# Kernel optimization log

Hardware: AMD Instinct MI355X
Metric: run time of the kernel (lower is better)

The kernel has to match this reference:

```python
import jax, jax.numpy as jnp
import numpy as np

B, D, C, F = 1024, 8192, 345, 512
PROTO_W = 0.99  # args.proto_m


def setup_inputs() -> dict:
    key = jax.random.key(0)
    k = jax.random.split(key, 6)
    img_q = jax.random.normal(k[0], (B, D), jnp.float32)
    img_q1 = jax.random.normal(k[1], (B, D), jnp.float32)
    # partial label mask: random candidate set, guarantee >=1 candidate per row
    partial_Y = (jax.random.uniform(k[2], (B, C)) < 0.3).astype(jnp.float32)
    partial_Y = partial_Y.at[jnp.arange(B), jnp.arange(B) % C].set(1.0)
    W_enc = jax.random.normal(k[3], (D, F), jnp.float32) / np.sqrt(D).astype(np.float32)
    W_fc = jax.random.normal(k[4], (F, C), jnp.float32) / np.sqrt(F).astype(np.float32)
    b_fc = jnp.zeros((C,), jnp.float32)
    proto = jax.random.normal(k[5], (C, F), jnp.float32)
    proto = proto / jnp.linalg.norm(proto, axis=1, keepdims=True)
    return {"img_q": img_q, "img_q1": img_q1, "partial_Y": partial_Y,
            "W_enc": W_enc, "W_fc": W_fc, "b_fc": b_fc, "proto": proto}


def reference(img_q, img_q1, partial_Y, W_enc, W_fc, b_fc, proto):
    # encoder: feats [B,F], logits [B,C] (abstracted backbone + shared fc)
    feats_q = img_q @ W_enc
    logits_q = feats_q @ W_fc + b_fc
    feats_q1 = img_q1 @ W_enc
    logits_q1 = feats_q1 @ W_fc + b_fc

    # partial-label restricted pseudo labels
    scores = jax.nn.softmax(logits_q, axis=1) * partial_Y
    scores = scores / scores.sum(axis=1, keepdims=True)
    labels = jnp.argmax(scores, axis=1)  # [B] int

    # Sequential per-sample EMA p[l] = w*p[l] + (1-w)*f, vectorized in closed form.
    # For a sample with c_after same-label samples occurring later, its final
    # contribution is (1-w)*w^c_after * f; the old prototype is scaled by w^count.
    onehot = jax.nn.one_hot(labels, C, dtype=feats_q.dtype)   # [B,C]
    cum = jnp.cumsum(onehot, axis=0)                          # inclusive counts
    occ = cum[jnp.arange(B), labels] - 1.0                    # occurrences before i
    total = cum[-1]                                           # [C] per-class counts
    c_after = total[labels] - occ - 1.0                       # [B]
    coef = (1.0 - PROTO_W) * PROTO_W ** c_after               # [B]
    contrib = jax.ops.segment_sum(coef[:, None] * feats_q, labels, num_segments=C)
    new_proto = (PROTO_W ** total)[:, None] * proto + contrib
    new_proto = new_proto / jnp.linalg.norm(new_proto, axis=1, keepdims=True)

    prot_scores = new_proto @ W_fc + b_fc
    return logits_q, logits_q1, new_proto, prot_scores, labels, feats_q, feats_q1
```

## Files before the change

### kernel.cpp

```cpp
#include <hip/hip_runtime.h>
#include <float.h>
#include <math.h>

#define B_SZ 1024
#define D_SZ 8192
#define C_SZ 345
#define F_SZ 512
#define PROTO_W 0.99f


#define WS_XH 0
#define WS_XL 33554432u
#define WS_WH 67108864u
#define WS_WL 75497472u
#define WS_P  83886080u
#define WS2_WFH 100663296u
#define WS2_WFL 101056512u
#define WS2_LAB 101449728u
#define WS2_NEED 101457920u

#define WS_NEED 92274688u
#define WS_FH  0u
#define WS_FL  2097152u
#define WS_WFH 4194304u
#define WS_WFL 4587520u
#define WS_NPH 4980736u
#define WS_NPL 5373952u

typedef short bf16x8 __attribute__((ext_vector_type(8)));
typedef short short4v __attribute__((ext_vector_type(4)));
typedef short short8v __attribute__((ext_vector_type(8)));
typedef float f32x4  __attribute__((ext_vector_type(4)));

__device__ __forceinline__ void split_bf16(float x, short& hi, short& lo) {
    unsigned u = __float_as_uint(x);
    unsigned r = (u + 0x7FFFu + ((u >> 16) & 1u)) >> 16;
    hi = (short)r;
    float hf = __uint_as_float(r << 16);
    lo = (short)(__float_as_uint(x - hf) >> 16);
}
__device__ __forceinline__ float bf16_f32(short h) {
    return __uint_as_float(((unsigned)(unsigned short)h) << 16);
}

__device__ __forceinline__ void gl_lds16(const short* g, short* l) {
    __builtin_amdgcn_global_load_lds(
        (const __attribute__((address_space(1))) void*)g,
        (__attribute__((address_space(3))) void*)l, 16, 0, 0);
}

__device__ __forceinline__ unsigned f2key(float v) {
    unsigned u = __float_as_uint(v);
    return (u & 0x80000000u) ? ~u : (u | 0x80000000u);
}

#define MFMA_BF16 __builtin_amdgcn_mfma_f32_16x16x32_bf16

#define MFMA_BLOCK(IA0, IA1, IB0, IB1)                                   \
    do {                                                                 \
        bf16x8 a0h = *(const bf16x8*)&sAh[IA0];                          \
        bf16x8 a1h = *(const bf16x8*)&sAh[IA1];                          \
        bf16x8 b0h = *(const bf16x8*)&sBh[IB0];                          \
        bf16x8 b1h = *(const bf16x8*)&sBh[IB1];                          \
        bf16x8 a0l = *(const bf16x8*)&sAl[IA0];                          \
        bf16x8 a1l = *(const bf16x8*)&sAl[IA1];                          \
        bf16x8 b0l = *(const bf16x8*)&sBl[IB0];                          \
        bf16x8 b1l = *(const bf16x8*)&sBl[IB1];                          \
        acc[0][0] = MFMA_BF16(a0h, b0h, acc[0][0], 0, 0, 0);             \
        acc[0][1] = MFMA_BF16(a0h, b1h, acc[0][1], 0, 0, 0);             \
        acc[1][0] = MFMA_BF16(a1h, b0h, acc[1][0], 0, 0, 0);             \
        acc[1][1] = MFMA_BF16(a1h, b1h, acc[1][1], 0, 0, 0);             \
        acc[0][0] = MFMA_BF16(a0h, b0l, acc[0][0], 0, 0, 0);             \
        acc[0][1] = MFMA_BF16(a0h, b1l, acc[0][1], 0, 0, 0);             \
        acc[1][0] = MFMA_BF16(a1h, b0l, acc[1][0], 0, 0, 0);             \
        acc[1][1] = MFMA_BF16(a1h, b1l, acc[1][1], 0, 0, 0);             \
        acc[0][0] = MFMA_BF16(a0l, b0h, acc[0][0], 0, 0, 0);             \
        acc[0][1] = MFMA_BF16(a0l, b1h, acc[0][1], 0, 0, 0);             \
        acc[1][0] = MFMA_BF16(a1l, b0h, acc[1][0], 0, 0, 0);             \
        acc[1][1] = MFMA_BF16(a1l, b1h, acc[1][1], 0, 0, 0);             \
    } while (0)

__global__ __launch_bounds__(256) void convert_all(
    const float* __restrict__ img_q, const float* __restrict__ img_q1,
    const float* __restrict__ W_enc, const float* __restrict__ W_fc,
    short* __restrict__ Xh, short* __restrict__ Xl,
    short* __restrict__ Wh, short* __restrict__ Wl,
    short* __restrict__ Wth, short* __restrict__ Wtl)
{
    __shared__ float tile[64][65];
    const int bid = blockIdx.x;
    const int t = threadIdx.x;

    if (bid < 1024) {
        const int HALF = (B_SZ * D_SZ) / 4;
        const int total = 2 * HALF;
        for (int i4 = bid * 256 + t; i4 < total; i4 += 1024 * 256) {
            float4 v = (i4 < HALF) ? ((const float4*)img_q)[i4]
                                   : ((const float4*)img_q1)[i4 - HALF];
            short4v h, l;
            short hh, ll;
            split_bf16(v.x, hh, ll); h.x = hh; l.x = ll;
            split_bf16(v.y, hh, ll); h.y = hh; l.y = ll;
            split_bf16(v.z, hh, ll); h.z = hh; l.z = ll;
            split_bf16(v.w, hh, ll); h.w = hh; l.w = ll;
            ((short4v*)Xh)[i4] = h;
            ((short4v*)Xl)[i4] = l;
        }
    } else if (bid < 2048) {
        const int id = bid - 1024;
        const int k0 = (id >> 3) * 64;
        const int n0 = (id & 7) * 64;
        {
            const int kr = t >> 2;
            const int cb = (t & 3) * 16;
#pragma unroll
            for (int j = 0; j < 4; ++j) {
                float4 v = *(const float4*)&W_enc[(size_t)(k0 + kr) * F_SZ + n0 + cb + j * 4];
                tile[kr][cb + j * 4 + 0] = v.x;
                tile[kr][cb + j * 4 + 1] = v.y;
                tile[kr][cb + j * 4 + 2] = v.z;
                tile[kr][cb + j * 4 + 3] = v.w;
            }
        }
        __syncthreads();
        const int n = t >> 2;
#pragma unroll
        for (int cc = 0; cc < 2; ++cc) {
            const int ch = (t & 3) * 2 + cc;
            short8v h, l;
#pragma unroll
            for (int e = 0; e < 8; ++e) {
                short hh, ll;
                split_bf16(tile[ch * 8 + e][n], hh, ll);
                h[e] = hh; l[e] = ll;
            }
            size_t off = (size_t)(n0 + n) * D_SZ + k0 + ch * 8;
            *(short8v*)&Wh[off] = h;
            *(short8v*)&Wl[off] = l;
        }
    } else {
        const int id = bid - 2048;
        const int k0 = (id & 7) * 64;
        const int c0 = (id >> 3) * 64;
        for (int idx = t; idx < 64 * 64; idx += 256) {
            const int kr = idx >> 6;
            const int cc = idx & 63;
            tile[kr][cc] = (c0 + cc < C_SZ) ? W_fc[(size_t)(k0 + kr) * C_SZ + c0 + cc] : 0.0f;
        }
        __syncthreads();
        const int crow = t >> 2;
#pragma unroll
        for (int cc2 = 0; cc2 < 2; ++cc2) {
            const int ch = (t & 3) * 2 + cc2;
            short8v h, l;
#pragma unroll
            for (int e = 0; e < 8; ++e) {
                short hh, ll;
                split_bf16(tile[ch * 8 + e][crow], hh, ll);
                h[e] = hh; l[e] = ll;
            }
            size_t off = (size_t)(c0 + crow) * F_SZ + k0 + ch * 8;
            *(short8v*)&Wth[off] = h;
            *(short8v*)&Wtl[off] = l;
        }
    }
}

__global__ __launch_bounds__(256, 1) void gemm_ws128(
    const short* __restrict__ Xh, const short* __restrict__ Xl,
    const short* __restrict__ Wh, const short* __restrict__ Wl,
    float* __restrict__ P, int ksteps)
{
    __shared__ __align__(16) short sAh[2][8192];
    __shared__ __align__(16) short sAl[2][8192];
    __shared__ __align__(16) short sBh[2][8192];
    __shared__ __align__(16) short sBl[2][8192];

    const int t = threadIdx.x;
    const int lane = t & 63;
    const int wave = t >> 6;
    const int nt = blockIdx.x;
    const int mt = blockIdx.y;
    const int ks = blockIdx.z;
    const int m0 = mt * 128;
    const int n0 = nt * 128;
    const int kbase = ks * ksteps * 64;

    const short* gbase =
        (wave == 0) ? Xh + (size_t)m0 * D_SZ :
        (wave == 1) ? Xl + (size_t)m0 * D_SZ :
        (wave == 2) ? Wh + (size_t)n0 * D_SZ :
                      Wl + (size_t)n0 * D_SZ;
    short* lb[2];
    lb[0] = (wave == 0) ? sAh[0] : (wave == 1) ? sAl[0] : (wave == 2) ? sBh[0] : sBl[0];
    lb[1] = (wave == 0) ? sAh[1] : (wave == 1) ? sAl[1] : (wave == 2) ? sBh[1] : sBl[1];
    const int lrow8 = lane >> 3;
    const int gchunkOff = ((lane & 7) ^ lrow8) * 8;
    const short* gsrc = gbase + (size_t)lrow8 * D_SZ + kbase + gchunkOff;

    const int mo = (wave >> 1) * 64;
    const int no = (wave & 1) * 64;
    const int lr = lane & 15;
    const int lkg = lane >> 4;
    const int x7 = lr & 7;
    const int sl0 = lkg ^ x7;
    const int sl1 = (4 + lkg) ^ x7;
    int aoff[4], boff[4];
#pragma unroll
    for (int f = 0; f < 4; ++f) {
        aoff[f] = (mo + 16 * f + lr) * 64;
        boff[f] = (no + 16 * f + lr) * 64;
    }

    f32x4 acc[4][4] = {};

#pragma unroll
    for (int j = 0; j < 16; ++j)
        gl_lds16(gsrc + (size_t)(8 * j) * D_SZ, lb[0] + j * 512);
    __syncthreads();

    int buf = 0;
    for (int s = 0; s < ksteps; ++s) {
        if (s + 1 < ksteps) {
            short* dst = lb[buf ^ 1];
            const short* g = gsrc + (s + 1) * 64;
#pragma unroll
            for (int j = 0; j < 16; ++j)
                gl_lds16(g + (size_t)(8 * j) * D_SZ, dst + j * 512);
        }
        const short* pAh = sAh[buf];
        const short* pAl = sAl[buf];
        const short* pBh = sBh[buf];
        const short* pBl = sBl[buf];
#pragma unroll
        for (int ksub = 0; ksub < 2; ++ksub) {
            const int sl = ksub ? sl1 : sl0;
            bf16x8 ah[4], al[4], bh[4], blo[4];
#pragma unroll
            for (int f = 0; f < 4; ++f) {
                ah[f]  = *(const bf16x8*)&pAh[aoff[f] + sl * 8];
                al[f]  = *(const bf16x8*)&pAl[aoff[f] + sl * 8];
            }
#pragma unroll
            for (int g = 0; g < 4; ++g) {
                bh[g]  = *(const bf16x8*)&pBh[boff[g] + sl * 8];
                blo[g] = *(const bf16x8*)&pBl[boff[g] + sl * 8];
            }
#pragma unroll
            for (int f = 0; f < 4; ++f)
#pragma unroll
                for (int g = 0; g < 4; ++g)
                    acc[f][g] = MFMA_BF16(ah[f], bh[g], acc[f][g], 0, 0, 0);
#pragma unroll
            for (int f = 0; f < 4; ++f)
#pragma unroll
                for (int g = 0; g < 4; ++g)
                    acc[f][g] = MFMA_BF16(ah[f], blo[g], acc[f][g], 0, 0, 0);
#pragma unroll
            for (int f = 0; f < 4; ++f)
#pragma unroll
                for (int g = 0; g < 4; ++g)
                    acc[f][g] = MFMA_BF16(al[f], bh[g], acc[f][g], 0, 0, 0);
        }
        __syncthreads();
        buf ^= 1;
    }

    float* Pout = P + (size_t)ks * (2048u * 512u);
#pragma unroll
    for (int f = 0; f < 4; ++f)
#pragma unroll
        for (int g = 0; g < 4; ++g) {
            const int col  = n0 + no + 16 * g + (lane & 15);
            const int row0 = m0 + mo + 16 * f + (lane >> 4) * 4;
#pragma unroll
            for (int r = 0; r < 4; ++r)
                Pout[(size_t)(row0 + r) * F_SZ + col] = acc[f][g][r];
        }
}

__global__ __launch_bounds__(256) void fc_logits_fused2(
    const float* __restrict__ P,
    const short* __restrict__ Bh_g, const short* __restrict__ Bl_g,
    const float* __restrict__ bias, const float* __restrict__ partial_Y,
    float* __restrict__ logits, float* __restrict__ feats,
    unsigned long long* __restrict__ labPack)
{
    __shared__ __align__(16) short sAh[4096];
    __shared__ __align__(16) short sAl[4096];
    __shared__ __align__(16) short sBh[4096];
    __shared__ __align__(16) short sBl[4096];

    const int t = threadIdx.x;
    const int lane = t & 63;
    const int wave = t >> 6;
    const int n0 = blockIdx.x * 64;
    const int m0 = blockIdx.y * 64;
    const bool writeF = (blockIdx.x == 0);

    const int lrow8 = lane >> 3;
    const int colOff = ((lane & 7) ^ lrow8) * 8;

    const int mo = (wave >> 1) * 32;
    const int no = (wave & 1) * 32;
    const int lr = lane & 15;
    const int lkg = lane >> 4;
    const int x7 = lr & 7;
    const int sl0 = (0 + lkg) ^ x7;
    const int sl1 = (4 + lkg) ^ x7;
    const int ra0 = (mo + lr) * 64,      ra1 = (mo + 16 + lr) * 64;
    const int rb0 = (no + lr) * 64,      rb1 = (no + 16 + lr) * 64;
    const int a00 = ra0 + sl0 * 8, a01 = ra0 + sl1 * 8;
    const int a10 = ra1 + sl0 * 8, a11 = ra1 + sl1 * 8;
    const int b00 = rb0 + sl0 * 8, b01 = rb0 + sl1 * 8;
    const int b10 = rb1 + sl0 * 8, b11 = rb1 + sl1 * 8;

    f32x4 acc[2][2] = {};

    for (int s = 0; s < 8; ++s) {
        __syncthreads();
        if (wave < 2) {
            const short* gB = (wave == 0) ? Bh_g : Bl_g;
            short* lbase = (wave == 0) ? sBh : sBl;
#pragma unroll
            for (int j = 0; j < 8; ++j) {
                int row = n0 + lrow8 + 8 * j;
                gl_lds16(gB + (size_t)row * F_SZ + s * 64 + colOff, lbase + j * 512);
            }
        }
#pragma unroll
        for (int qq = 0; qq < 2; ++qq) {
            const int q = t + qq * 256;
            const int row = q >> 3;
            const int c = q & 7;
            const size_t gidx = (size_t)(m0 + row) * F_SZ + s * 64 + c * 8;
            float4 v0 = ((const float4*)&P[gidx])[0];
            float4 v1 = ((const float4*)&P[gidx])[1];
#pragma unroll
            for (int sl = 1; sl < 4; ++sl) {
                const float* Ps = P + (size_t)sl * (2048u * 512u);
                float4 u0 = ((const float4*)&Ps[gidx])[0];
                float4 u1 = ((const float4*)&Ps[gidx])[1];
                v0.x += u0.x; v0.y += u0.y; v0.z += u0.z; v0.w += u0.w;
                v1.x += u1.x; v1.y += u1.y; v1.z += u1.z; v1.w += u1.w;
            }
            float f[8] = {v0.x, v0.y, v0.z, v0.w, v1.x, v1.y, v1.z, v1.w};
            if (writeF) {
#pragma unroll
                for (int e = 0; e < 8; ++e) feats[gidx + e] = f[e];
            }
            bf16x8 h, l;
#pragma unroll
            for (int e = 0; e < 8; ++e) { short hh, ll; split_bf16(f[e], hh, ll); h[e] = hh; l[e] = ll; }
            const int slot = c ^ (row & 7);
            *(bf16x8*)&sAh[row * 64 + slot * 8] = h;
            *(bf16x8*)&sAl[row * 64 + slot * 8] = l;
        }
        __syncthreads();
        MFMA_BLOCK(a00, a10, b00, b10);
        MFMA_BLOCK(a01, a11, b01, b11);
    }

    const bool doArg = (m0 < B_SZ);
#pragma unroll
    for (int f = 0; f < 2; ++f) {
#pragma unroll
        for (int r = 0; r < 4; ++r) {
            const int row = m0 + mo + f * 16 + (lane >> 4) * 4 + r;
            unsigned long long best = 0;
#pragma unroll
            for (int g = 0; g < 2; ++g) {
                const int col = n0 + no + g * 16 + (lane & 15);
                if (col < C_SZ) {
                    const float v = acc[f][g][r] + bias[col];
                    logits[(size_t)row * C_SZ + col] = v;
                    if (doArg && partial_Y[(size_t)row * C_SZ + col] != 0.0f) {
                        unsigned long long p = ((unsigned long long)f2key(v) << 32)
                                             | (unsigned long long)(0xFFFFFFFFu - (unsigned)col);
                        if (p > best) best = p;
                    }
                }
            }
            if (doArg) {
#pragma unroll
                for (int m = 1; m < 16; m <<= 1) {
                    unsigned long long o = __shfl_xor(best, m);
                    if (o > best) best = o;
                }
                if ((lane & 15) == 0 && best != 0)
                    atomicMax(&labPack[row], best);
            }
        }
    }
}

__global__ __launch_bounds__(512) void proto_scores_fused(
    const unsigned long long* __restrict__ labPack,
    const float* __restrict__ feats_q,
    const float* __restrict__ proto,
    const short* __restrict__ Wth, const short* __restrict__ Wtl,
    const float* __restrict__ b_fc,
    float* __restrict__ new_proto, float* __restrict__ scores,
    float* __restrict__ labels_f)
{
    __shared__ int rowlist[B_SZ];
    __shared__ int mcount_s;
    __shared__ float nprow[F_SZ];
    __shared__ float red[8];
    __shared__ float rinv_s;
    const int c = blockIdx.x;
    const int t = threadIdx.x;
    const int lane = t & 63;
    const int w = t >> 6;

    if (c == 0) {
#pragma unroll
        for (int j = 0; j < 2; ++j) {
            const int i = t + j * 512;
            int li = (int)(0xFFFFFFFFu - (unsigned)(labPack[i] & 0xFFFFFFFFull));
            labels_f[i] = (float)li;
        }
    }

    if (w == 0) {
        int k = 0;
#pragma unroll
        for (int ch = 0; ch < 16; ++ch) {
            unsigned long long pk = labPack[ch * 64 + lane];
            int li = (int)(0xFFFFFFFFu - (unsigned)(pk & 0xFFFFFFFFull));
            unsigned long long mask = __ballot(li == c);
            if (lane == 0) {
                while (mask) {
                    int p = __builtin_ctzll(mask);
                    mask &= mask - 1;
                    rowlist[k++] = ch * 64 + p;
                }
            }
            k = __shfl(k, 0);
        }
        if (lane == 0) mcount_s = k;
    }
    __syncthreads();
    const int m = mcount_s;

    float val = proto[(size_t)c * F_SZ + t];
    for (int k = 0; k < m; ++k)
        val = PROTO_W * val + (1.0f - PROTO_W) * feats_q[(size_t)rowlist[k] * F_SZ + t];

    float sq = val * val;
#pragma unroll
    for (int off = 32; off; off >>= 1) sq += __shfl_down(sq, off);
    if ((t & 63) == 0) red[t >> 6] = sq;
    __syncthreads();
    if (t == 0) {
        float s = 0.0f;
#pragma unroll
        for (int ww = 0; ww < 8; ++ww) s += red[ww];
        rinv_s = 1.0f / sqrtf(s);
    }
    __syncthreads();
    const float v = val * rinv_s;
    new_proto[(size_t)c * F_SZ + t] = v;
    nprow[t] = v;
    __syncthreads();

    float np8[8];
#pragma unroll
    for (int j = 0; j < 8; ++j) np8[j] = nprow[lane * 8 + j];
    for (int col = w; col < C_SZ; col += 8) {
        const short8v h = *(const short8v*)&Wth[(size_t)col * F_SZ + lane * 8];
        const short8v l = *(const short8v*)&Wtl[(size_t)col * F_SZ + lane * 8];
        float p = 0.0f;
#pragma unroll
        for (int j = 0; j < 8; ++j)
            p += np8[j] * (bf16_f32(h[j]) + bf16_f32(l[j]));
#pragma unroll
        for (int off = 32; off; off >>= 1) p += __shfl_down(p, off);
        if (lane == 0) scores[(size_t)c * C_SZ + col] = p + b_fc[col];
    }
}

__global__ __launch_bounds__(256) void reduce_feats_split(
    const float* __restrict__ P, float* __restrict__ feats,
    short* __restrict__ Fh, short* __restrict__ Fl,
    const float* __restrict__ W_fc,
    short* __restrict__ Wth, short* __restrict__ Wtl)
{
    const int bid = blockIdx.x;
    const int t = threadIdx.x;
    if (bid < 1024) {
        const int n4 = (2048 * 512) / 4;
        const float* P1 = P + 2048 * 512;
        for (int i4 = bid * 256 + t; i4 < n4; i4 += 1024 * 256) {
            float4 a = ((const float4*)P)[i4];
            float4 b = ((const float4*)P1)[i4];
            float v[4] = {a.x + b.x, a.y + b.y, a.z + b.z, a.w + b.w};
            short4v h, l;
            short hh, ll;
#pragma unroll
            for (int e = 0; e < 4; ++e) {
                feats[i4 * 4 + e] = v[e];
                split_bf16(v[e], hh, ll); h[e] = hh; l[e] = ll;
            }
            ((short4v*)Fh)[i4] = h;
            ((short4v*)Fl)[i4] = l;
        }
    } else {
        __shared__ float tile[64][65];
        const int id = bid - 1024;
        const int k0 = (id & 7) * 64;
        const int c0 = (id >> 3) * 64;
        for (int idx = t; idx < 64 * 64; idx += 256) {
            const int kr = idx >> 6;
            const int cc = idx & 63;
            tile[kr][cc] = (c0 + cc < C_SZ) ? W_fc[(size_t)(k0 + kr) * C_SZ + c0 + cc] : 0.0f;
        }
        __syncthreads();
        const int crow = t >> 2;
#pragma unroll
        for (int cc2 = 0; cc2 < 2; ++cc2) {
            const int ch = (t & 3) * 2 + cc2;
            short8v h, l;
#pragma unroll
            for (int e = 0; e < 8; ++e) {
                short hh, ll;
                split_bf16(tile[ch * 8 + e][crow], hh, ll);
                h[e] = hh; l[e] = ll;
            }
            size_t off = (size_t)(c0 + crow) * F_SZ + k0 + ch * 8;
            *(short8v*)&Wth[off] = h;
            *(short8v*)&Wtl[off] = l;
        }
    }
}

__global__ __launch_bounds__(256) void gemm_fc(
    const short* __restrict__ Ah, const short* __restrict__ Al,
    const short* __restrict__ Bh, const short* __restrict__ Bl,
    const float* __restrict__ bias, float* __restrict__ Cout, int M)
{
    __shared__ __align__(16) short sAh[4096];
    __shared__ __align__(16) short sAl[4096];
    __shared__ __align__(16) short sBh[4096];
    __shared__ __align__(16) short sBl[4096];

    const int t = threadIdx.x;
    const int lane = t & 63;
    const int wave = t >> 6;
    const int n0 = blockIdx.x * 64;
    const int m0 = blockIdx.y * 64;

    const int lrow8 = lane >> 3;
    const int colOff = ((lane & 7) ^ lrow8) * 8;

    short* lbase = (wave == 0) ? sAh : (wave == 1) ? sAl : (wave == 2) ? sBh : sBl;
    const short* gA = (wave == 1) ? Al : Ah;
    const short* gB = (wave == 3) ? Bl : Bh;
    const bool isA = wave < 2;

    const int mo = (wave >> 1) * 32;
    const int no = (wave & 1) * 32;
    const int lr = lane & 15;
    const int lkg = lane >> 4;
    const int x7 = lr & 7;
    const int sl0 = (0 + lkg) ^ x7;
    const int sl1 = (4 + lkg) ^ x7;
    const int ra0 = (mo + lr) * 64,      ra1 = (mo + 16 + lr) * 64;
    const int rb0 = (no + lr) * 64,      rb1 = (no + 16 + lr) * 64;
    const int a00 = ra0 + sl0 * 8, a01 = ra0 + sl1 * 8;
    const int a10 = ra1 + sl0 * 8, a11 = ra1 + sl1 * 8;
    const int b00 = rb0 + sl0 * 8, b01 = rb0 + sl1 * 8;
    const int b10 = rb1 + sl0 * 8, b11 = rb1 + sl1 * 8;

    f32x4 acc[2][2] = {};

    for (int s = 0; s < 8; ++s) {
        __syncthreads();
        if (isA) {
#pragma unroll
            for (int j = 0; j < 8; ++j) {
                int row = m0 + lrow8 + 8 * j;
                if (row > M - 1) row = M - 1;
                gl_lds16(gA + (size_t)row * F_SZ + s * 64 + colOff, lbase + j * 512);
            }
        } else {
#pragma unroll
            for (int j = 0; j < 8; ++j) {
                int row = n0 + lrow8 + 8 * j;
                gl_lds16(gB + (size_t)row * F_SZ + s * 64 + colOff, lbase + j * 512);
            }
        }
        __syncthreads();
        MFMA_BLOCK(a00, a10, b00, b10);
        MFMA_BLOCK(a01, a11, b01, b11);
    }

#pragma unroll
    for (int f = 0; f < 2; ++f)
#pragma unroll
        for (int g = 0; g < 2; ++g) {
            const int col  = n0 + no + g * 16 + (lane & 15);
            if (col >= C_SZ) continue;
            const float bb = bias[col];
            const int row0 = m0 + mo + f * 16 + (lane >> 4) * 4;
#pragma unroll
            for (int r = 0; r < 4; ++r) {
                const int row = row0 + r;
                if (row < M)
                    Cout[(size_t)row * C_SZ + col] = acc[f][g][r] + bb;
            }
        }
}

__global__ __launch_bounds__(64) void argmax_labels(
    const float* __restrict__ logits, const float* __restrict__ partial_Y,
    float* __restrict__ labels_f)
{
    const int i = blockIdx.x;
    const int lane = threadIdx.x;
    float best = -FLT_MAX;
    int bidx = C_SZ;
    for (int c = lane; c < C_SZ; c += 64) {
        if (partial_Y[(size_t)i * C_SZ + c] != 0.0f) {
            float v = logits[(size_t)i * C_SZ + c];
            if (v > best || (v == best && c < bidx)) { best = v; bidx = c; }
        }
    }
#pragma unroll
    for (int off = 32; off; off >>= 1) {
        float ov = __shfl_down(best, off);
        int oi = __shfl_down(bidx, off);
        if (ov > best || (ov == best && oi < bidx)) { best = ov; bidx = oi; }
    }
    if (lane == 0) labels_f[i] = (float)bidx;
}

__global__ __launch_bounds__(512) void proto_update(
    const float* __restrict__ labels_f, const float* __restrict__ feats_q,
    const float* __restrict__ proto, float* __restrict__ new_proto,
    short* __restrict__ NPh, short* __restrict__ NPl)
{
    __shared__ int lab[B_SZ];
    __shared__ float red[8];
    __shared__ float rinv_s;
    const int c = blockIdx.x;
    const int t = threadIdx.x;
    for (int i = t; i < B_SZ; i += 512) lab[i] = (int)labels_f[i];
    __syncthreads();
    float val = proto[(size_t)c * F_SZ + t];
    for (int i = 0; i < B_SZ; ++i) {
        if (lab[i] == c)
            val = PROTO_W * val + (1.0f - PROTO_W) * feats_q[(size_t)i * F_SZ + t];
    }
    float sq = val * val;
#pragma unroll
    for (int off = 32; off; off >>= 1) sq += __shfl_down(sq, off);
    if ((t & 63) == 0) red[t >> 6] = sq;
    __syncthreads();
    if (t == 0) {
        float s = 0.0f;
#pragma unroll
        for (int w = 0; w < 8; ++w) s += red[w];
        rinv_s = 1.0f / sqrtf(s);
    }
    __syncthreads();
    const float v = val * rinv_s;
    new_proto[(size_t)c * F_SZ + t] = v;
    if (NPh) {
        short hh, ll;
        split_bf16(v, hh, ll);
        NPh[(size_t)c * F_SZ + t] = hh;
        NPl[(size_t)c * F_SZ + t] = ll;
    }
}

extern "C" void kernel_launch(void* const* d_in, const int* in_sizes, int n_in,
                              void* d_out, int out_size, void* d_ws, size_t ws_size,
                              hipStream_t stream)
{
    const float* img_q     = (const float*)d_in[0];
    const float* img_q1    = (const float*)d_in[1];
    const float* partial_Y = (const float*)d_in[2];
    const float* W_enc     = (const float*)d_in[3];
    const float* W_fc      = (const float*)d_in[4];
    const float* b_fc      = (const float*)d_in[5];
    const float* proto     = (const float*)d_in[6];

    float* out       = (float*)d_out;
    float* logits    = out;
    float* new_proto = out + 706560;
    float* scores    = out + 883200;
    float* labels_f  = out + 1002225;
    float* feats     = out + 1003249;

    char* ws = (char*)d_ws;
    short* Xh = (short*)(ws + WS_XH);
    short* Xl = (short*)(ws + WS_XL);
    short* Wh = (short*)(ws + WS_WH);
    short* Wl = (short*)(ws + WS_WL);
    float* P  = (float*)(ws + WS_P);

    if (ws_size >= (size_t)WS2_NEED) {
        short* Wth = (short*)(ws + WS2_WFH);
        short* Wtl = (short*)(ws + WS2_WFL);
        unsigned long long* labPack = (unsigned long long*)(ws + WS2_LAB);

        hipMemsetAsync(labPack, 0, B_SZ * sizeof(unsigned long long), stream);
        hipLaunchKernelGGL(convert_all, dim3(2096), dim3(256), 0, stream,
                           img_q, img_q1, W_enc, W_fc, Xh, Xl, Wh, Wl, Wth, Wtl);
        hipLaunchKernelGGL(gemm_ws128, dim3(4, 16, 4), dim3(256), 0, stream,
                           Xh, Xl, Wh, Wl, P, 32);
        hipLaunchKernelGGL(fc_logits_fused2, dim3(6, 32), dim3(256), 0, stream,
                           P, Wth, Wtl, b_fc, partial_Y, logits, feats, labPack);
        hipLaunchKernelGGL(proto_scores_fused, dim3(345), dim3(512), 0, stream,
                           labPack, feats, proto, Wth, Wtl, b_fc,
                           new_proto, scores, labels_f);
    } else {
        short* Fh  = (short*)(ws + WS_FH);
        short* Fl  = (short*)(ws + WS_FL);
        short* Wth = (short*)(ws + WS_WFH);
        short* Wtl = (short*)(ws + WS_WFL);
        short* NPh = (short*)(ws + WS_NPH);
        short* NPl = (short*)(ws + WS_NPL);

        hipLaunchKernelGGL(convert_all, dim3(2048), dim3(256), 0, stream,
                           img_q, img_q1, W_enc, W_fc, Xh, Xl, Wh, Wl,
                           (short*)nullptr, (short*)nullptr);
        hipLaunchKernelGGL(gemm_ws128, dim3(4, 16, 2), dim3(256), 0, stream,
                           Xh, Xl, Wh, Wl, P, 64);
        hipLaunchKernelGGL(reduce_feats_split, dim3(1072), dim3(256), 0, stream,
                           P, feats, Fh, Fl, W_fc, Wth, Wtl);
        hipLaunchKernelGGL(gemm_fc, dim3(6, 32), dim3(256), 0, stream,
                           Fh, Fl, Wth, Wtl, b_fc, logits, 2048);
        hipLaunchKernelGGL(argmax_labels, dim3(1024), dim3(64), 0, stream,
                           logits, partial_Y, labels_f);
        hipLaunchKernelGGL(proto_update, dim3(345), dim3(512), 0, stream,
                           labels_f, feats, proto, new_proto, NPh, NPl);
        hipLaunchKernelGGL(gemm_fc, dim3(6, 6), dim3(256), 0, stream,
                           NPh, NPl, Wth, Wtl, b_fc, scores, C_SZ);
    }
}
```

Measured before the change: 257.1 us.

## Split out split-K reduction and double-buffer the fc GEMM with async LDS loads

Moves the split-K partial-sum reduction and bf16 hi/lo split into a separate reduce_feats4 kernel. Previously every column block of the fc kernel re-read and re-summed all four partial slices of P. The new fc_logits3 kernel streams precomputed Fh/Fl tiles with global-to-LDS loads into double buffers. The main split-K GEMM swaps __syncthreads for explicit vmcnt waits plus raw barriers and raises wave priority around the MFMA section, so prefetch overlaps compute. This costs one extra kernel launch and a 4 MB round-trip through workspace, and it doubles LDS use in the fc kernel.

```diff
diff --git a/kernel.cpp b/kernel.cpp
--- a/kernel.cpp
+++ b/kernel.cpp
@@ -18,6 +18,8 @@
 #define WS2_WFL 101056512u
 #define WS2_LAB 101449728u
 #define WS2_NEED 101457920u
+#define WS2_FH 0u
+#define WS2_FL 2097152u
 
 #define WS_NEED 92274688u
 #define WS_FH  0u
@@ -52,6 +54,12 @@
 __device__ __forceinline__ unsigned f2key(float v) {
     unsigned u = __float_as_uint(v);
     return (u & 0x80000000u) ? ~u : (u | 0x80000000u);
+}
+
+__device__ __forceinline__ void fence_barrier() {
+    asm volatile("" ::: "memory");
+    __builtin_amdgcn_s_barrier();
+    asm volatile("" ::: "memory");
 }
 
 #define MFMA_BF16 __builtin_amdgcn_mfma_f32_16x16x32_bf16
@@ -217,7 +225,6 @@
 #pragma unroll
     for (int j = 0; j < 16; ++j)
         gl_lds16(gsrc + (size_t)(8 * j) * D_SZ, lb[0] + j * 512);
-    __syncthreads();
 
     int buf = 0;
     for (int s = 0; s < ksteps; ++s) {
@@ -227,42 +234,51 @@
 #pragma unroll
             for (int j = 0; j < 16; ++j)
                 gl_lds16(g + (size_t)(8 * j) * D_SZ, dst + j * 512);
-        }
-        const short* pAh = sAh[buf];
-        const short* pAl = sAl[buf];
-        const short* pBh = sBh[buf];
-        const short* pBl = sBl[buf];
-#pragma unroll
-        for (int ksub = 0; ksub < 2; ++ksub) {
-            const int sl = ksub ? sl1 : sl0;
-            bf16x8 ah[4], al[4], bh[4], blo[4];
-#pragma unroll
-            for (int f = 0; f < 4; ++f) {
-                ah[f]  = *(const bf16x8*)&pAh[aoff[f] + sl * 8];
-                al[f]  = *(const bf16x8*)&pAl[aoff[f] + sl * 8];
-            }
-#pragma unroll
-            for (int g = 0; g < 4; ++g) {
-                bh[g]  = *(const bf16x8*)&pBh[boff[g] + sl * 8];
-                blo[g] = *(const bf16x8*)&pBl[boff[g] + sl * 8];
-            }
-#pragma unroll
-            for (int f = 0; f < 4; ++f)
-#pragma unroll
-                for (int g = 0; g < 4; ++g)
-                    acc[f][g] = MFMA_BF16(ah[f], bh[g], acc[f][g], 0, 0, 0);
-#pragma unroll
-            for (int f = 0; f < 4; ++f)
-#pragma unroll
-                for (int g = 0; g < 4; ++g)
-                    acc[f][g] = MFMA_BF16(ah[f], blo[g], acc[f][g], 0, 0, 0);
-#pragma unroll
-            for (int f = 0; f < 4; ++f)
-#pragma unroll
-                for (int g = 0; g < 4; ++g)
-                    acc[f][g] = MFMA_BF16(al[f], bh[g], acc[f][g], 0, 0, 0);
-        }
-        __syncthreads();
+            asm volatile("s_waitcnt vmcnt(16)" ::: "memory");
+        } else {
+            asm volatile("s_waitcnt vmcnt(0)" ::: "memory");
+        }
+        fence_barrier();
+
+        __builtin_amdgcn_s_setprio(1);
+        {
+            const short* pAh = sAh[buf];
+            const short* pAl = sAl[buf];
+            const short* pBh = sBh[buf];
+            const short* pBl = sBl[buf];
+#pragma unroll
+            for (int ksub = 0; ksub < 2; ++ksub) {
+                const int sl = ksub ? sl1 : sl0;
+                bf16x8 ah[4], al[4], bh[4], blo[4];
+#pragma unroll
+                for (int f = 0; f < 4; ++f) {
+                    ah[f]  = *(const bf16x8*)&pAh[aoff[f] + sl * 8];
+                    al[f]  = *(const bf16x8*)&pAl[aoff[f] + sl * 8];
+                }
+#pragma unroll
+                for (int g = 0; g < 4; ++g) {
+                    bh[g]  = *(const bf16x8*)&pBh[boff[g] + sl * 8];
+                    blo[g] = *(const bf16x8*)&pBl[boff[g] + sl * 8];
+                }
+#pragma unroll
+                for (int f = 0; f < 4; ++f)
+#pragma unroll
+                    for (int g = 0; g < 4; ++g)
+                        acc[f][g] = MFMA_BF16(ah[f], bh[g], acc[f][g], 0, 0, 0);
+#pragma unroll
+                for (int f = 0; f < 4; ++f)
+#pragma unroll
+                    for (int g = 0; g < 4; ++g)
+                        acc[f][g] = MFMA_BF16(ah[f], blo[g], acc[f][g], 0, 0, 0);
+#pragma unroll
+                for (int f = 0; f < 4; ++f)
+#pragma unroll
+                    for (int g = 0; g < 4; ++g)
+                        acc[f][g] = MFMA_BF16(al[f], bh[g], acc[f][g], 0, 0, 0);
+            }
+        }
+        __builtin_amdgcn_s_setprio(0);
+        fence_barrier();
         buf ^= 1;
     }
 
@@ -279,27 +295,56 @@
         }
 }
 
-__global__ __launch_bounds__(256) void fc_logits_fused2(
-    const float* __restrict__ P,
+__global__ __launch_bounds__(256) void reduce_feats4(
+    const float* __restrict__ P, float* __restrict__ feats,
+    short* __restrict__ Fh, short* __restrict__ Fl)
+{
+    const int i4 = blockIdx.x * 256 + threadIdx.x;
+    float4 a = ((const float4*)P)[i4];
+#pragma unroll
+    for (int sl = 1; sl < 4; ++sl) {
+        float4 b = ((const float4*)(P + (size_t)sl * (2048u * 512u)))[i4];
+        a.x += b.x; a.y += b.y; a.z += b.z; a.w += b.w;
+    }
+    ((float4*)feats)[i4] = a;
+    float v[4] = {a.x, a.y, a.z, a.w};
+    short4v h, l;
+    short hh, ll;
+#pragma unroll
+    for (int e = 0; e < 4; ++e) {
+        split_bf16(v[e], hh, ll); h[e] = hh; l[e] = ll;
+    }
+    ((short4v*)Fh)[i4] = h;
+    ((short4v*)Fl)[i4] = l;
+}
+
+__global__ __launch_bounds__(256, 2) void fc_logits3(
+    const short* __restrict__ Ah, const short* __restrict__ Al,
     const short* __restrict__ Bh_g, const short* __restrict__ Bl_g,
     const float* __restrict__ bias, const float* __restrict__ partial_Y,
-    float* __restrict__ logits, float* __restrict__ feats,
-    unsigned long long* __restrict__ labPack)
-{
-    __shared__ __align__(16) short sAh[4096];
-    __shared__ __align__(16) short sAl[4096];
-    __shared__ __align__(16) short sBh[4096];
-    __shared__ __align__(16) short sBl[4096];
+    float* __restrict__ logits, unsigned long long* __restrict__ labPack)
+{
+    __shared__ __align__(16) short dAh[2][4096];
+    __shared__ __align__(16) short dAl[2][4096];
+    __shared__ __align__(16) short dBh[2][4096];
+    __shared__ __align__(16) short dBl[2][4096];
 
     const int t = threadIdx.x;
     const int lane = t & 63;
     const int wave = t >> 6;
     const int n0 = blockIdx.x * 64;
     const int m0 = blockIdx.y * 64;
-    const bool writeF = (blockIdx.x == 0);
 
     const int lrow8 = lane >> 3;
     const int colOff = ((lane & 7) ^ lrow8) * 8;
+
+    const short* gsrc = (wave == 0) ? Ah : (wave == 1) ? Al
+                      : (wave == 2) ? Bh_g : Bl_g;
+    const int rbase = (wave < 2) ? m0 : n0;
+    short* lb[2];
+    lb[0] = (wave == 0) ? dAh[0] : (wave == 1) ? dAl[0] : (wave == 2) ? dBh[0] : dBl[0];
+    lb[1] = (wave == 0) ? dAh[1] : (wave == 1) ? dAl[1] : (wave == 2) ? dBh[1] : dBl[1];
+    const short* gbase = gsrc + (size_t)(rbase + lrow8) * F_SZ + colOff;
 
     const int mo = (wave >> 1) * 32;
     const int no = (wave & 1) * 32;
@@ -317,48 +362,35 @@
 
     f32x4 acc[2][2] = {};
 
+#pragma unroll
+    for (int j = 0; j < 8; ++j)
+        gl_lds16(gbase + (size_t)(8 * j) * F_SZ, lb[0] + j * 512);
+
+    int buf = 0;
     for (int s = 0; s < 8; ++s) {
-        __syncthreads();
-        if (wave < 2) {
-            const short* gB = (wave == 0) ? Bh_g : Bl_g;
-            short* lbase = (wave == 0) ? sBh : sBl;
-#pragma unroll
-            for (int j = 0; j < 8; ++j) {
-                int row = n0 + lrow8 + 8 * j;
-                gl_lds16(gB + (size_t)row * F_SZ + s * 64 + colOff, lbase + j * 512);
-            }
-        }
-#pragma unroll
-        for (int qq = 0; qq < 2; ++qq) {
-            const int q = t + qq * 256;
-            const int row = q >> 3;
-            const int c = q & 7;
-            const size_t gidx = (size_t)(m0 + row) * F_SZ + s * 64 + c * 8;
-            float4 v0 = ((const float4*)&P[gidx])[0];
-            float4 v1 = ((const float4*)&P[gidx])[1];
-#pragma unroll
-            for (int sl = 1; sl < 4; ++sl) {
-                const float* Ps = P + (size_t)sl * (2048u * 512u);
-                float4 u0 = ((const float4*)&Ps[gidx])[0];
-                float4 u1 = ((const float4*)&Ps[gidx])[1];
-                v0.x += u0.x; v0.y += u0.y; v0.z += u0.z; v0.w += u0.w;
-                v1.x += u1.x; v1.y += u1.y; v1.z += u1.z; v1.w += u1.w;
-            }
-            float f[8] = {v0.x, v0.y, v0.z, v0.w, v1.x, v1.y, v1.z, v1.w};
-            if (writeF) {
-#pragma unroll
-                for (int e = 0; e < 8; ++e) feats[gidx + e] = f[e];
-            }
-            bf16x8 h, l;
-#pragma unroll
-            for (int e = 0; e < 8; ++e) { short hh, ll; split_bf16(f[e], hh, ll); h[e] = hh; l[e] = ll; }
-            const int slot = c ^ (row & 7);
-            *(bf16x8*)&sAh[row * 64 + slot * 8] = h;
-            *(bf16x8*)&sAl[row * 64 + slot * 8] = l;
-        }
-        __syncthreads();
-        MFMA_BLOCK(a00, a10, b00, b10);
-        MFMA_BLOCK(a01, a11, b01, b11);
+        if (s + 1 < 8) {
+            short* dst = lb[buf ^ 1];
+            const short* g = gbase + (s + 1) * 64;
+#pragma unroll
+            for (int j = 0; j < 8; ++j)
+                gl_lds16(g + (size_t)(8 * j) * F_SZ, dst + j * 512);
+            asm volatile("s_waitcnt vmcnt(8)" ::: "memory");
+        } else {
+            asm volatile("s_waitcnt vmcnt(0)" ::: "memory");
+        }
+        fence_barrier();
+        __builtin_amdgcn_s_setprio(1);
+        {
+            const short* sAh = dAh[buf];
+            const short* sAl = dAl[buf];
+            const short* sBh = dBh[buf];
+            const short* sBl = dBl[buf];
+            MFMA_BLOCK(a00, a10, b00, b10);
+            MFMA_BLOCK(a01, a11, b01, b11);
+        }
+        __builtin_amdgcn_s_setprio(0);
+        fence_barrier();
+        buf ^= 1;
     }
 
     const bool doArg = (m0 < B_SZ);
@@ -704,14 +736,18 @@
         short* Wth = (short*)(ws + WS2_WFH);
         short* Wtl = (short*)(ws + WS2_WFL);
         unsigned long long* labPack = (unsigned long long*)(ws + WS2_LAB);
+        short* Fh = (short*)(ws + WS2_FH);
+        short* Fl = (short*)(ws + WS2_FL);
 
         hipMemsetAsync(labPack, 0, B_SZ * sizeof(unsigned long long), stream);
         hipLaunchKernelGGL(convert_all, dim3(2096), dim3(256), 0, stream,
                            img_q, img_q1, W_enc, W_fc, Xh, Xl, Wh, Wl, Wth, Wtl);
         hipLaunchKernelGGL(gemm_ws128, dim3(4, 16, 4), dim3(256), 0, stream,
                            Xh, Xl, Wh, Wl, P, 32);
-        hipLaunchKernelGGL(fc_logits_fused2, dim3(6, 32), dim3(256), 0, stream,
-                           P, Wth, Wtl, b_fc, partial_Y, logits, feats, labPack);
+        hipLaunchKernelGGL(reduce_feats4, dim3(1024), dim3(256), 0, stream,
+                           P, feats, Fh, Fl);
+        hipLaunchKernelGGL(fc_logits3, dim3(6, 32), dim3(256), 0, stream,
+                           Fh, Fl, Wth, Wtl, b_fc, partial_Y, logits, labPack);
         hipLaunchKernelGGL(proto_scores_fused, dim3(345), dim3(512), 0, stream,
                            labPack, feats, proto, Wth, Wtl, b_fc,
                            new_proto, scores, labels_f);
```

Result: faster. 250.1 us (-2.7%).
